# Kernel tuning notes

Measured on AMD Instinct MI355X. Metric: run time of the kernel, lower is better.

Reference implementation:

```python
import jax, jax.numpy as jnp
import numpy as np

D_MODEL, N_LEVELS, N_HEADS, N_POINTS = 256, 4, 8, 4
HEAD_DIM = D_MODEL // N_HEADS
SPATIAL = [(100, 100), (50, 50), (25, 25), (13, 13)]  # (H, W) per level
BATCH = 2


def setup_inputs() -> dict:
    key = jax.random.key(0)
    ks = jax.random.split(key, 10)
    len_in = sum(h * w for h, w in SPATIAL)
    n, lq = BATCH, len_in
    s = 0.02
    mlp = N_HEADS * N_LEVELS * N_POINTS
    starts = np.cumsum([0] + [h * w for h, w in SPATIAL])[:-1]
    return {
        "query": jax.random.normal(ks[0], (n, lq, D_MODEL), jnp.float32),
        "reference_points": jax.random.uniform(ks[1], (n, lq, N_LEVELS, 2), jnp.float32),
        "input_flatten": jax.random.normal(ks[2], (n, len_in, D_MODEL), jnp.float32),
        "input_spatial_shapes": jnp.array(SPATIAL, dtype=jnp.int32),
        "input_level_start_index": jnp.array(starts, dtype=jnp.int32),
        "Wv": jax.random.normal(ks[3], (D_MODEL, D_MODEL), jnp.float32) * s,
        "bv": jnp.zeros((D_MODEL,), jnp.float32),
        "Woff": jax.random.normal(ks[4], (D_MODEL, mlp * 2), jnp.float32) * s,
        "boff": jax.random.normal(ks[5], (mlp * 2,), jnp.float32) * s,
        "Wattn": jax.random.normal(ks[6], (D_MODEL, mlp), jnp.float32) * s,
        "battn": jnp.zeros((mlp,), jnp.float32),
        "Wout": jax.random.normal(ks[7], (D_MODEL, D_MODEL), jnp.float32) * s,
        "bout": jnp.zeros((D_MODEL,), jnp.float32),
    }


def _ms_deform_attn_core(value, spatial_shapes, loc, aw):
    """value [N,S,M,D]; loc [N,Lq,M,L,P,2] in [0,1]; aw [N,Lq,M,L,P] -> [N,Lq,M*D].
    Faithful to F.grid_sample(mode='bilinear', padding_mode='zeros', align_corners=False)."""
    n, lq, m, L, p, _ = loc.shape
    d = value.shape[-1]
    out = jnp.zeros((n, m, lq, d), value.dtype)
    gather = jax.vmap(jax.vmap(lambda v, i: v[i]))  # vmap over N and M
    start = 0
    for lvl, (H, W) in enumerate(spatial_shapes):
        v = value[:, start:start + H * W].transpose(0, 2, 1, 3)  # [N,M,HW,D]
        start += H * W
        # align_corners=False: grid g=2*loc-1 -> pixel = ((g+1)*size-1)/2 = loc*size-0.5
        x = loc[:, :, :, lvl, :, 0] * W - 0.5  # [N,Lq,M,P]
        y = loc[:, :, :, lvl, :, 1] * H - 0.5
        x0 = jnp.floor(x)
        y0 = jnp.floor(y)
        wx = x - x0
        wy = y - y0
        x0i = x0.astype(jnp.int32)
        y0i = y0.astype(jnp.int32)
        samp = jnp.zeros((n, m, lq * p, d), value.dtype)
        for dy, wyc in ((0, 1.0 - wy), (1, wy)):
            for dx, wxc in ((0, 1.0 - wx), (1, wx)):
                xi = x0i + dx
                yi = y0i + dy
                valid = (xi >= 0) & (xi < W) & (yi >= 0) & (yi < H)  # zeros padding
                idx = jnp.clip(yi, 0, H - 1) * W + jnp.clip(xi, 0, W - 1)
                idx = idx.transpose(0, 2, 1, 3).reshape(n, m, lq * p)
                w = (wxc * wyc * valid).transpose(0, 2, 1, 3).reshape(n, m, lq * p)
                samp = samp + gather(v, idx) * w[..., None]
        samp = samp.reshape(n, m, lq, p, d)
        aw_l = aw[:, :, :, lvl, :].transpose(0, 2, 1, 3)  # [N,M,Lq,P]
        out = out + (samp * aw_l[..., None]).sum(3)
    return out.transpose(0, 2, 1, 3).reshape(n, lq, m * d)


def reference(query, reference_points, input_flatten, input_spatial_shapes,
              input_level_start_index, Wv, bv, Woff, boff, Wattn, battn, Wout, bout):
    n, lq, _ = query.shape
    m, L, p = N_HEADS, N_LEVELS, N_POINTS
    shapes = np.asarray(input_spatial_shapes)  # concrete/static [L,2] = (H,W)
    value = (input_flatten @ Wv + bv).reshape(n, -1, m, HEAD_DIM)
    off = (query @ Woff + boff).reshape(n, lq, m, L, p, 2)
    aw = jax.nn.softmax((query @ Wattn + battn).reshape(n, lq, m, L * p), axis=-1)
    aw = aw.reshape(n, lq, m, L, p)
    norm = jnp.asarray(shapes[:, ::-1].astype(np.float32))  # [L,2] = (W,H)
    loc = reference_points[:, :, None, :, None, :] + off / norm[None, None, None, :, None, :]
    out = _ms_deform_attn_core(value, [tuple(s) for s in shapes.tolist()], loc, aw)
    return out @ Wout + bout
```

## Files before the change

### kernel.cpp

```cpp
#include <hip/hip_runtime.h>
#include <hip/hip_bf16.h>

#define NB    2
#define LQ    13294
#define DM    256
#define NH    8
#define HD    32
#define NL    4
#define NP    4
#define ROWS  (NB*LQ)

#define OFF_VALUE 0u
#define OFF_TMP   13613056u
#define OFF_OFFS  27226112u
#define OFF_AWL   54452224u
#define OFF_WT    61258752u
#define OFF_FLAG  61717504u

#define WT_WV    0
#define WT_WOFF  65536
#define WT_WATTN 131072
#define WT_WOUT  163840

typedef __attribute__((ext_vector_type(8))) short short8;
typedef __attribute__((ext_vector_type(4))) float floatx4;

static __device__ __forceinline__ float blo(int u)  { return __uint_as_float(((unsigned)u) << 16); }
static __device__ __forceinline__ float bhif(int u) { return __uint_as_float(((unsigned)u) & 0xffff0000u); }

static __device__ __forceinline__ int pack_bf2(float a, float b) {
    __hip_bfloat162 h(__float2bfloat16(a), __float2bfloat16(b));
    int u; __builtin_memcpy(&u, &h, 4); return u;
}

__global__ void sniff_k(const unsigned int* __restrict__ q, int* __restrict__ flag) {
    const int t = threadIdx.x;
    int hits = 0;
#pragma unroll
    for (int i = 0; i < 4; ++i) {
        unsigned lo = q[t * 4 + i] & 0xffffu;
        unsigned e  = (lo >> 7) & 0xffu;
        if ((e >= 110u && e <= 132u) || lo == 0u) ++hits;
    }
#pragma unroll
    for (int s = 1; s < 64; s <<= 1) hits += __shfl_xor(hits, s);
    if (t == 0) *flag = (hits > 160) ? 1 : 0;
}

__global__ __launch_bounds__(256) void trans_k(
    const void* __restrict__ s0, const void* __restrict__ s1,
    const void* __restrict__ s2, const void* __restrict__ s3,
    short* __restrict__ wt, const int* __restrict__ flagp)
{
    const int flag = *flagp;
    const int z = blockIdx.z;
    const void* src = (z == 0) ? s0 : (z == 1) ? s1 : (z == 2) ? s2 : s3;
    short* dst = wt + ((z == 0) ? WT_WV : (z == 1) ? WT_WOFF : (z == 2) ? WT_WATTN : WT_WOUT);
    const int N = (z == 2) ? 128 : 256;
    const int n0 = blockIdx.x * 32, k0 = blockIdx.y * 32;
    if (n0 >= N) return;

    __shared__ short tile[32 * 36];
    const int t = threadIdx.x;
    const int r = t >> 3, c4 = (t & 7) * 4;
    if (flag) {
        const short* sp = (const short*)src + (k0 + r) * N + n0 + c4;
        *(short4*)&tile[r * 36 + c4] = *(const short4*)sp;
    } else {
        const float* sp = (const float*)src + (k0 + r) * N + n0 + c4;
        float4 v = *(const float4*)sp;
        short4 o;
        o.x = (short)(pack_bf2(v.x, v.x) & 0xffff);
        o.y = (short)(pack_bf2(v.y, v.y) & 0xffff);
        o.z = (short)(pack_bf2(v.z, v.z) & 0xffff);
        o.w = (short)(pack_bf2(v.w, v.w) & 0xffff);
        *(short4*)&tile[r * 36 + c4] = o;
    }
    __syncthreads();
    const int nn = t >> 3, r4 = (t & 7) * 4;
    short4 o;
    o.x = tile[(r4 + 0) * 36 + nn];
    o.y = tile[(r4 + 1) * 36 + nn];
    o.z = tile[(r4 + 2) * 36 + nn];
    o.w = tile[(r4 + 3) * 36 + nn];
    *(short4*)&dst[(n0 + nn) * 256 + k0 + r4] = o;
}

static __device__ __forceinline__ short8 ldA_f32(const float* p) {
    float4 f0 = *(const float4*)p, f1 = *(const float4*)(p + 4);
    int4 q; q.x = pack_bf2(f0.x, f0.y); q.y = pack_bf2(f0.z, f0.w);
            q.z = pack_bf2(f1.x, f1.y); q.w = pack_bf2(f1.z, f1.w);
    short8 r; __builtin_memcpy(&r, &q, 16); return r;
}

__global__ __launch_bounds__(64) void wgemm_k(
    const void* __restrict__ A, const short* __restrict__ Wt,
    const void* __restrict__ bias, const void* __restrict__ bias2,
    void* __restrict__ C, void* __restrict__ C2,
    int M, int Nn, int a_mode, int c_mode, const int* __restrict__ flagp)
{
    const int flag = *flagp;
    const bool a_bf = (a_mode == 1) || (flag != 0);
    const int lane = threadIdx.x;
    const int qd = lane >> 4, ln = lane & 15;
    const int bm = blockIdx.y * 32, bn = blockIdx.x * 64;

    const int ar0 = min(bm + ln, M - 1);
    const int ar1 = min(bm + 16 + ln, M - 1);
    const short* Ab = (const short*)A;
    const float* Af = (const float*)A;

    floatx4 acc[2][4];
#pragma unroll
    for (int i = 0; i < 2; ++i)
#pragma unroll
        for (int j = 0; j < 4; ++j) acc[i][j] = floatx4{0.f, 0.f, 0.f, 0.f};

    if (a_bf) {
#pragma unroll 2
        for (int kk = 0; kk < 8; ++kk) {
            const int k0 = kk * 32 + qd * 8;
            short8 af0 = *(const short8*)(Ab + ar0 * 256 + k0);
            short8 af1 = *(const short8*)(Ab + ar1 * 256 + k0);
            short8 bf[4];
#pragma unroll
            for (int j = 0; j < 4; ++j)
                bf[j] = *(const short8*)(Wt + (bn + j * 16 + ln) * 256 + k0);
#pragma unroll
            for (int j = 0; j < 4; ++j) {
                acc[0][j] = __builtin_amdgcn_mfma_f32_16x16x32_bf16(af0, bf[j], acc[0][j], 0, 0, 0);
                acc[1][j] = __builtin_amdgcn_mfma_f32_16x16x32_bf16(af1, bf[j], acc[1][j], 0, 0, 0);
            }
        }
    } else {
#pragma unroll 2
        for (int kk = 0; kk < 8; ++kk) {
            const int k0 = kk * 32 + qd * 8;
            short8 af0 = ldA_f32(Af + ar0 * 256 + k0);
            short8 af1 = ldA_f32(Af + ar1 * 256 + k0);
            short8 bf[4];
#pragma unroll
            for (int j = 0; j < 4; ++j)
                bf[j] = *(const short8*)(Wt + (bn + j * 16 + ln) * 256 + k0);
#pragma unroll
            for (int j = 0; j < 4; ++j) {
                acc[0][j] = __builtin_amdgcn_mfma_f32_16x16x32_bf16(af0, bf[j], acc[0][j], 0, 0, 0);
                acc[1][j] = __builtin_amdgcn_mfma_f32_16x16x32_bf16(af1, bf[j], acc[1][j], 0, 0, 0);
            }
        }
    }

#pragma unroll
    for (int j = 0; j < 4; ++j) {
        const int col = bn + j * 16 + ln;
        float bj;
        if (c_mode == 3 && col >= 256) {
            if (flag) bj = __bfloat162float(((const __hip_bfloat16*)bias2)[col - 256]);
            else      bj = ((const float*)bias2)[col - 256];
        } else {
            if (flag) bj = __bfloat162float(((const __hip_bfloat16*)bias)[col]);
            else      bj = ((const float*)bias)[col];
        }
#pragma unroll
        for (int i = 0; i < 2; ++i) {
#pragma unroll
            for (int r = 0; r < 4; ++r) {
                const int row = bm + i * 16 + qd * 4 + r;
                if (row >= M) continue;
                const float v = acc[i][j][r] + bj;
                if (c_mode == 0)      ((__hip_bfloat16*)C)[row * Nn + col] = __float2bfloat16(v);
                else if (c_mode == 1) ((float*)C)[row * Nn + col] = v;
                else if (c_mode == 2) {
                    if (flag) ((__hip_bfloat16*)C)[row * Nn + col] = __float2bfloat16(v);
                    else      ((float*)C)[row * Nn + col] = v;
                } else {
                    if (col < 256) ((float*)C)[row * 256 + col] = v;
                    else           ((__hip_bfloat16*)C2)[row * 128 + col - 256] = __float2bfloat16(v);
                }
            }
        }
    }
}

__global__ __launch_bounds__(256) void sampler_k(
    const void* __restrict__ refp, const short* __restrict__ value,
    const float* __restrict__ offs, const short* __restrict__ awl,
    short* __restrict__ tmp, const int* __restrict__ flagp)
{
    const int flag = *flagp;
    const int wq = threadIdx.x >> 6;
    const int nq = blockIdx.x * 4 + wq;
    const int lane = threadIdx.x & 63;
    const int h = lane >> 3, u = lane & 7;
    const int n = (nq >= LQ) ? 1 : 0;

    __shared__ int2 recs[4][16][9][5];

    const int lg = *(const int*)(awl + nq * 128 + h * 16 + u * 2);
    float l0 = blo(lg), l1 = bhif(lg);
    float m = fmaxf(l0, l1);
    m = fmaxf(m, __shfl_xor(m, 1));
    m = fmaxf(m, __shfl_xor(m, 2));
    m = fmaxf(m, __shfl_xor(m, 4));
    float e0 = __expf(l0 - m), e1 = __expf(l1 - m);
    float s = e0 + e1;
    s += __shfl_xor(s, 1);
    s += __shfl_xor(s, 2);
    s += __shfl_xor(s, 4);
    const float inv = 1.f / s;
    const float w0 = e0 * inv, w1 = e1 * inv;

    const float4 of = *(const float4*)(offs + nq * 256 + h * 32 + u * 4);

    float rxl, ryl;
    if (flag) {
        const int rr = *(const int*)((const short*)refp + nq * 8 + (u & 3) * 2);
        rxl = blo(rr); ryl = bhif(rr);
    } else {
        const float* rp = (const float*)refp + nq * 8 + (u & 3) * 2;
        rxl = rp[0]; ryl = rp[1];
    }

    const int l = u >> 1;
    const int Wl = (0x0D193264 >> (l * 8)) & 0xff;
    const int St = (l == 0) ? 0 : (l == 1) ? 10000 : (l == 2) ? 12500 : 13125;
    const int rowbase = n * LQ + St;
    const float Wf = (float)Wl;
    const float rx = __shfl(rxl, h * 8 + l);
    const float ry = __shfl(ryl, h * 8 + l);

#pragma unroll
    for (int j = 0; j < 2; ++j) {
        const float ox = j ? of.z : of.x;
        const float oy = j ? of.w : of.y;
        const float wa = j ? w1 : w0;
        const float px = fmaf(rx, Wf, ox) - 0.5f;
        const float py = fmaf(ry, Wf, oy) - 0.5f;
        const float x0f = floorf(px), y0f = floorf(py);
        const float wx = px - x0f, wy = py - y0f;
        const int x0 = (int)x0f, y0 = (int)y0f;
        const float wxc[2] = {1.f - wx, wx};
        const float wyc[2] = {1.f - wy, wy};
#pragma unroll
        for (int dy = 0; dy < 2; ++dy) {
#pragma unroll
            for (int dx = 0; dx < 2; ++dx) {
                const int xi = x0 + dx, yi = y0 + dy;
                const bool vld = ((unsigned)xi < (unsigned)Wl) & ((unsigned)yi < (unsigned)Wl);
                int row = rowbase + yi * Wl + xi;
                row = vld ? row : rowbase;
                recs[wq][u * 2 + j][h][dy * 2 + dx] =
                    make_int2(row << 9, __float_as_int(vld ? wa * wxc[dx] * wyc[dy] : 0.f));
            }
        }
    }

    __syncthreads();

    const int laneoff = h * 64 + u * 8;
    const char* vb = (const char*)value;
    float a0 = 0.f, a1 = 0.f, a2 = 0.f, a3 = 0.f;

    int2  rA[8], rB[8];
    float wA[8], wB[8];

#define CHUNK(RW, WW, kk)                                                 \
    _Pragma("unroll")                                                     \
    for (int j = 0; j < 8; ++j) {                                         \
        const int2 rr = recs[wq][(kk) * 2 + (j >> 2)][h][j & 3];          \
        WW[j] = __int_as_float(rr.y);                                     \
        RW[j] = *(const int2*)(vb + (unsigned)(rr.x + laneoff));          \
    }
#define EAT(RW, WW)                                                       \
    _Pragma("unroll")                                                     \
    for (int j = 0; j < 8; ++j) {                                         \
        a0 = fmaf(WW[j], blo(RW[j].x),  a0);                              \
        a1 = fmaf(WW[j], bhif(RW[j].x), a1);                              \
        a2 = fmaf(WW[j], blo(RW[j].y),  a2);                              \
        a3 = fmaf(WW[j], bhif(RW[j].y), a3);                              \
    }

    CHUNK(rA, wA, 0)
    CHUNK(rB, wB, 1)
    EAT(rA, wA)  CHUNK(rA, wA, 2)
    EAT(rB, wB)  CHUNK(rB, wB, 3)
    EAT(rA, wA)  CHUNK(rA, wA, 4)
    EAT(rB, wB)  CHUNK(rB, wB, 5)
    EAT(rA, wA)  CHUNK(rA, wA, 6)
    EAT(rB, wB)  CHUNK(rB, wB, 7)
    EAT(rA, wA)
    EAT(rB, wB)
#undef CHUNK
#undef EAT

    int2 o;
    o.x = pack_bf2(a0, a1);
    o.y = pack_bf2(a2, a3);
    *(int2*)(tmp + nq * 256 + h * 32 + u * 4) = o;
}

extern "C" void kernel_launch(void* const* d_in, const int* in_sizes, int n_in,
                              void* d_out, int out_size, void* d_ws, size_t ws_size,
                              hipStream_t stream)
{
    const void* query  = d_in[0];
    const void* refpts = d_in[1];
    const void* flat   = d_in[2];
    const void* Wv     = d_in[5];
    const void* bv     = d_in[6];
    const void* Woff   = d_in[7];
    const void* boff   = d_in[8];
    const void* Wattn  = d_in[9];
    const void* battn  = d_in[10];
    const void* Wout   = d_in[11];
    const void* bout   = d_in[12];

    char* ws = (char*)d_ws;
    short* value = (short*)(ws + OFF_VALUE);
    short* tmp   = (short*)(ws + OFF_TMP);
    float* offsb = (float*)(ws + OFF_OFFS);
    short* awl   = (short*)(ws + OFF_AWL);
    short* wt    = (short*)(ws + OFF_WT);
    int*   flagp = (int*)(ws + OFF_FLAG);

    const int mt = (ROWS + 31) / 32;

    sniff_k<<<1, 64, 0, stream>>>((const unsigned int*)query, flagp);
    trans_k<<<dim3(8, 8, 4), 256, 0, stream>>>(Wv, Woff, Wattn, Wout, wt, flagp);
    wgemm_k<<<dim3(4, mt), 64, 0, stream>>>(flat, wt + WT_WV, bv, nullptr,
                                            value, nullptr, ROWS, 256, 2, 0, flagp);
    wgemm_k<<<dim3(6, mt), 64, 0, stream>>>(query, wt + WT_WOFF, boff, battn,
                                            offsb, awl, ROWS, 384, 2, 3, flagp);
    sampler_k<<<ROWS / 4, 256, 0, stream>>>(refpts, value, offsb, awl, tmp, flagp);
    wgemm_k<<<dim3(4, mt), 64, 0, stream>>>(tmp, wt + WT_WOUT, bout, nullptr,
                                            d_out, nullptr, ROWS, 256, 1, 2, flagp);
}
```

Before: 283.2 us.

## Merge input projection GEMMs into one launch with XCD-aware block swizzle

The value projection and the offset/attention projection GEMMs now run as one kernel launch, with blocks split between the two jobs by index. Block indices are also remapped so consecutive tiles land on the same XCD, which should improve L2 reuse of weight and input panels. The output GEMM uses the same swizzle and compile-time specialised modes. This saves one launch and its tail, at the cost of more branching in the kernel and heterogeneous blocks sharing one grid.

```diff
diff --git a/kernel.cpp b/kernel.cpp
--- a/kernel.cpp
+++ b/kernel.cpp
@@ -22,6 +22,11 @@
 #define WT_WATTN 131072
 #define WT_WOUT  163840
 
+#define NPANEL   831
+#define NBLK_VAL (NPANEL*4)
+#define NBLK_FUS (NPANEL*6)
+#define NBLK_IN  (NBLK_VAL+NBLK_FUS)
+
 typedef __attribute__((ext_vector_type(8))) short short8;
 typedef __attribute__((ext_vector_type(4))) float floatx4;
 
@@ -31,6 +36,12 @@
 static __device__ __forceinline__ int pack_bf2(float a, float b) {
     __hip_bfloat162 h(__float2bfloat16(a), __float2bfloat16(b));
     int u; __builtin_memcpy(&u, &h, 4); return u;
+}
+
+static __device__ __forceinline__ int xcd_swz(int b, int nblk) {
+    const int q = nblk >> 3, r = nblk & 7;
+    const int x = b & 7, i = b >> 3;
+    return x * q + min(x, r) + i;
 }
 
 __global__ void sniff_k(const unsigned int* __restrict__ q, int* __restrict__ flag) {
@@ -93,17 +104,16 @@
     short8 r; __builtin_memcpy(&r, &q, 16); return r;
 }
 
-__global__ __launch_bounds__(64) void wgemm_k(
+static __device__ __forceinline__ void wgemm_body(
     const void* __restrict__ A, const short* __restrict__ Wt,
     const void* __restrict__ bias, const void* __restrict__ bias2,
     void* __restrict__ C, void* __restrict__ C2,
-    int M, int Nn, int a_mode, int c_mode, const int* __restrict__ flagp)
-{
-    const int flag = *flagp;
-    const bool a_bf = (a_mode == 1) || (flag != 0);
+    const int M, const int Nn, const bool a_bf, const int c_mode,
+    const int flag, const int bn_t, const int p_t)
+{
     const int lane = threadIdx.x;
     const int qd = lane >> 4, ln = lane & 15;
-    const int bm = blockIdx.y * 32, bn = blockIdx.x * 64;
+    const int bm = p_t * 32, bn = bn_t * 64;
 
     const int ar0 = min(bm + ln, M - 1);
     const int ar1 = min(bm + 16 + ln, M - 1);
@@ -182,6 +192,38 @@
     }
 }
 
+__global__ __launch_bounds__(64) void wgemm_in_k(
+    const void* __restrict__ flat, const void* __restrict__ query,
+    const short* __restrict__ wt,
+    const void* __restrict__ bv, const void* __restrict__ boff,
+    const void* __restrict__ battn,
+    void* __restrict__ value, void* __restrict__ offsb, void* __restrict__ awl,
+    const int* __restrict__ flagp)
+{
+    const int flag = *flagp;
+    const bool a_bf = (flag != 0);
+    const int w = xcd_swz(blockIdx.x, NBLK_IN);
+    if (w < NBLK_VAL) {
+        wgemm_body(flat, wt + WT_WV, bv, nullptr, value, nullptr,
+                   ROWS, 256, a_bf, 0, flag, w & 3, w >> 2);
+    } else {
+        const int w2 = w - NBLK_VAL;
+        wgemm_body(query, wt + WT_WOFF, boff, battn, offsb, awl,
+                   ROWS, 384, a_bf, 3, flag, w2 % 6, w2 / 6);
+    }
+}
+
+__global__ __launch_bounds__(64) void wgemm_out_k(
+    const void* __restrict__ tmp, const short* __restrict__ wt,
+    const void* __restrict__ bout, void* __restrict__ dout,
+    const int* __restrict__ flagp)
+{
+    const int flag = *flagp;
+    const int w = xcd_swz(blockIdx.x, NBLK_VAL);
+    wgemm_body(tmp, wt + WT_WOUT, bout, nullptr, dout, nullptr,
+               ROWS, 256, true, 2, flag, w & 3, w >> 2);
+}
+
 __global__ __launch_bounds__(256) void sampler_k(
     const void* __restrict__ refp, const short* __restrict__ value,
     const float* __restrict__ offs, const short* __restrict__ awl,
@@ -323,15 +365,10 @@
     short* wt    = (short*)(ws + OFF_WT);
     int*   flagp = (int*)(ws + OFF_FLAG);
 
-    const int mt = (ROWS + 31) / 32;
-
     sniff_k<<<1, 64, 0, stream>>>((const unsigned int*)query, flagp);
     trans_k<<<dim3(8, 8, 4), 256, 0, stream>>>(Wv, Woff, Wattn, Wout, wt, flagp);
-    wgemm_k<<<dim3(4, mt), 64, 0, stream>>>(flat, wt + WT_WV, bv, nullptr,
-                                            value, nullptr, ROWS, 256, 2, 0, flagp);
-    wgemm_k<<<dim3(6, mt), 64, 0, stream>>>(query, wt + WT_WOFF, boff, battn,
-                                            offsb, awl, ROWS, 384, 2, 3, flagp);
+    wgemm_in_k<<<NBLK_IN, 64, 0, stream>>>(flat, query, wt, bv, boff, battn,
+                                           value, offsb, awl, flagp);
     sampler_k<<<ROWS / 4, 256, 0, stream>>>(refpts, value, offsb, awl, tmp, flagp);
-    wgemm_k<<<dim3(4, mt), 64, 0, stream>>>(tmp, wt + WT_WOUT, bout, nullptr,
-                                            d_out, nullptr, ROWS, 256, 1, 2, flagp);
-}
+    wgemm_out_k<<<NBLK_VAL, 64, 0, stream>>>(tmp, wt, bout, d_out, flagp);
+}
```

Result: faster. 271.8 us (-4.0%).
